# Performance work log

Measured on AMD Instinct MI355X. Metric: run time of the kernel, lower is better.

## Reference

```python
import jax, jax.numpy as jnp
import numpy as np

H = 8        # num_heads
D = 768      # d_model
DH = D // H  # d_head = 96


def setup_inputs() -> dict:
    key = jax.random.key(0)
    ks = jax.random.split(key, 12)
    B, S = 4, 2048
    s_in = 1.0 / np.sqrt(D)
    s_cat = 1.0 / np.sqrt(D)
    return {
        "input_querys": jax.random.normal(ks[0], (B, S, D), jnp.float32),
        "input_key": jax.random.normal(ks[1], (B, S, D), jnp.float32),
        "input_values": jax.random.normal(ks[2], (B, S, D), jnp.float32),
        # per-head projection weights, stacked over the head axis
        "Wq": jax.random.normal(ks[3], (H, D, DH), jnp.float32) * s_in,
        "bq": jax.random.normal(ks[4], (H, DH), jnp.float32) * s_in,
        "Wk": jax.random.normal(ks[5], (H, D, DH), jnp.float32) * s_in,
        "bk": jax.random.normal(ks[6], (H, DH), jnp.float32) * s_in,
        "Wv": jax.random.normal(ks[7], (H, D, DH), jnp.float32) * s_in,
        "bv": jax.random.normal(ks[8], (H, DH), jnp.float32) * s_in,
        # output linear: (H*DH) -> D
        "Wo": jax.random.normal(ks[9], (H * DH, D), jnp.float32) * s_cat,
        "bo": jax.random.normal(ks[10], (D,), jnp.float32) * s_cat,
    }


def reference(input_querys, input_key, input_values, Wq, bq, Wk, bk, Wv, bv, Wo, bo):
    # Per-head linear projections (vectorized over the head axis)
    # q/k/v: [B,S,D] -> [B,H,S,DH]
    Q = jnp.einsum("bsd,hdk->bhsk", input_querys, Wq) + bq[None, :, None, :]
    K = jnp.einsum("bsd,hdk->bhsk", input_key, Wk) + bk[None, :, None, :]
    V = jnp.einsum("bsd,hdk->bhsk", input_values, Wv) + bv[None, :, None, :]

    scale = 1.0 / jnp.sqrt(jnp.asarray(DH, Q.dtype))
    scores = jnp.einsum("bhsk,bhtk->bhst", Q, K) * scale  # [B,H,S,S]
    attn = jax.nn.softmax(scores, axis=-1)
    out = jnp.einsum("bhst,bhtk->bhsk", attn, V)  # [B,H,S,DH]

    # concat heads (head-major order matches torch.cat over ModuleList)
    B, _, S, _ = out.shape
    cat = out.transpose(0, 2, 1, 3).reshape(B, S, H * DH)
    return cat @ Wo + bo
```

## Files before the change

### kernel.cpp

```cpp
#include <hip/hip_runtime.h>


typedef unsigned short u16;
typedef _Float16 h16;
typedef h16 h16x8 __attribute__((ext_vector_type(8)));
typedef __fp16 fp16x2 __attribute__((ext_vector_type(2)));
typedef __fp16 fp16x4 __attribute__((ext_vector_type(4)));
typedef unsigned short u16x8 __attribute__((ext_vector_type(8)));
typedef unsigned short u16x4 __attribute__((ext_vector_type(4)));
typedef float f32x4 __attribute__((ext_vector_type(4)));

__device__ __forceinline__ u16 f2h(float f) {
  union { h16 h; u16 u; } c; c.h = (h16)f; return c.u;
}

__device__ __forceinline__ void gll16(const void* g, void* l) {
  __builtin_amdgcn_global_load_lds(
      (const __attribute__((address_space(1))) void*)g,
      (__attribute__((address_space(3))) void*)l, 16, 0, 0);
}

__global__ __launch_bounds__(256) void prep_kernel(
    const float* __restrict__ Wq, const float* __restrict__ Wk,
    const float* __restrict__ Wv, const float* __restrict__ Wo,
    const float* __restrict__ Xk, const float* __restrict__ Xv,
    const float* __restrict__ Xq,
    u16* __restrict__ WqT, u16* __restrict__ WkT,
    u16* __restrict__ WvT, u16* __restrict__ WoT,
    u16* __restrict__ Xk16, u16* __restrict__ Xv16, u16* __restrict__ Xq16)
{
  const int bid = blockIdx.x;
  const int tid = threadIdx.x;

  if (bid >= 432) {
    const int i = bid - 432;
    const int t = i / 3072;
    const long e = ((long)(i % 3072) * 256 + tid) * 8;
    const float* src = (t == 0) ? Xk : (t == 1) ? Xv : Xq;
    u16* dst = (t == 0) ? Xk16 : (t == 1) ? Xv16 : Xq16;
    f32x4 a = *(const f32x4*)(&src[e]);
    f32x4 b = *(const f32x4*)(&src[e + 4]);
    u16x8 v;
    #pragma unroll
    for (int j = 0; j < 4; j++) { v[j] = f2h(a[j]); v[4 + j] = f2h(b[j]); }
    *(u16x8*)(&dst[e]) = v;
    return;
  }

  if (bid < 288) {
    __shared__ u16 Lt[96][72];
    const int w = bid / 96;
    const int r = bid % 96;
    const int h = r / 12, dt = r % 12;
    const float* W = (w == 0) ? Wq : (w == 1) ? Wk : Wv;
    u16* T = (w == 0) ? WqT : (w == 1) ? WkT : WvT;
    const float* src = W + (size_t)h * 73728 + (size_t)dt * 64 * 96;
    #pragma unroll
    for (int p = 0; p < 6; p++) {
      const int lin = p * 1024 + tid * 4;
      f32x4 v = *(const f32x4*)(&src[lin]);
      const int d = lin / 96, kk = lin % 96;
      #pragma unroll
      for (int j = 0; j < 4; j++) Lt[kk + j][d] = f2h(v[j]);
    }
    __syncthreads();
    #pragma unroll
    for (int c = 0; c < 3; c++) {
      const int ch = c * 256 + tid;
      const int kk = ch >> 3, dc = ch & 7;
      u16x8 o = *(const u16x8*)(&Lt[kk][dc * 8]);
      *(u16x8*)(&T[(size_t)(h * 96 + kk) * 768 + dt * 64 + dc * 8]) = o;
    }
    return;
  }

  {
    __shared__ u16 Lo[64][72];
    const int i = bid - 288;
    const int kt = i / 12, nt = i % 12;
    const float* src = Wo + (size_t)(kt * 64) * 768 + nt * 64;
    #pragma unroll
    for (int p = 0; p < 4; p++) {
      const int lin = p * 1024 + tid * 4;
      const int kr = lin >> 6, nc = lin & 63;
      f32x4 v = *(const f32x4*)(&src[(size_t)kr * 768 + nc]);
      #pragma unroll
      for (int j = 0; j < 4; j++) Lo[nc + j][kr] = f2h(v[j]);
    }
    __syncthreads();
    #pragma unroll
    for (int c = 0; c < 2; c++) {
      const int ch = c * 256 + tid;
      const int nr = ch >> 3, kc = ch & 7;
      u16x8 o = *(const u16x8*)(&Lo[nr][kc * 8]);
      *(u16x8*)(&WoT[(size_t)(nt * 64 + nr) * 768 + kt * 64 + kc * 8]) = o;
    }
  }
}

#define GK 768

__global__ __launch_bounds__(256) void gemm_qkv(
    const u16* __restrict__ Xq16, const u16* __restrict__ Xk16,
    const u16* __restrict__ Xv16, const u16* __restrict__ WT,
    const float* __restrict__ bq, const float* __restrict__ bk,
    const float* __restrict__ bv,
    u16* __restrict__ Q16, u16* __restrict__ K16, u16* __restrict__ VT)
{
  const int z = blockIdx.z;
  const u16* BT = WT + (size_t)z * 589824;
  const float* bias = (z == 0) ? bq : (z == 1) ? bk : bv;
  const u16* A = (z == 0) ? Xq16 : (z == 1) ? Xk16 : Xv16;

  __shared__ __align__(16) u16 As[128 * 32];
  __shared__ __align__(16) u16 Bs[128 * 32];
  const int tid = threadIdx.x;
  const int wave = tid >> 6;
  const int lane = tid & 63;
  const int quad = lane >> 4;
  const int l16 = lane & 15;
  const int m0 = blockIdx.x * 128;
  const int n0 = blockIdx.y * 128;

  f32x4 acc[2][8];
  #pragma unroll
  for (int i = 0; i < 2; i++)
    #pragma unroll
    for (int j = 0; j < 8; j++) acc[i][j] = (f32x4){0.f, 0.f, 0.f, 0.f};

  const int Lr = lane >> 2, Lc = (lane & 3) * 8;
  const u16* gA0 = A + (size_t)(m0 + wave * 32 + Lr) * GK + Lc;
  const u16* gA1 = gA0 + (size_t)16 * GK;
  const u16* gB0 = BT + (size_t)(n0 + wave * 32 + Lr) * GK + Lc;
  const u16* gB1 = gB0 + (size_t)16 * GK;
  u16* lA0 = &As[(wave * 32) * 32];
  u16* lA1 = &As[(wave * 32 + 16) * 32];
  u16* lB0 = &Bs[(wave * 32) * 32];
  u16* lB1 = &Bs[(wave * 32 + 16) * 32];

  for (int kt = 0; kt < 24; kt++) {
    gll16(gA0, lA0);
    gll16(gA1, lA1);
    gll16(gB0, lB0);
    gll16(gB1, lB1);
    gA0 += 32; gA1 += 32; gB0 += 32; gB1 += 32;
    __syncthreads();

    h16x8 af[2], bf[8];
    #pragma unroll
    for (int mf = 0; mf < 2; mf++)
      af[mf] = *(const h16x8*)(&As[(wave * 32 + mf * 16 + l16) * 32 + quad * 8]);
    #pragma unroll
    for (int nf = 0; nf < 8; nf++)
      bf[nf] = *(const h16x8*)(&Bs[(nf * 16 + l16) * 32 + quad * 8]);
    #pragma unroll
    for (int mf = 0; mf < 2; mf++)
      #pragma unroll
      for (int nf = 0; nf < 8; nf++)
        acc[mf][nf] = __builtin_amdgcn_mfma_f32_16x16x32_f16(af[mf], bf[nf], acc[mf][nf], 0, 0, 0);
    __syncthreads();
  }

  u16* Yr = (z == 0) ? Q16 : K16;
  #pragma unroll
  for (int nf = 0; nf < 8; nf++) {
    const int n = n0 + nf * 16 + l16;
    const float bv2 = bias[n];
    #pragma unroll
    for (int mf = 0; mf < 2; mf++) {
      const int m = m0 + wave * 32 + mf * 16 + quad * 4;
      if (z == 2) {
        const int b = m >> 11, s = m & 2047;
        u16x4 pk;
        #pragma unroll
        for (int r = 0; r < 4; r++) pk[r] = f2h(acc[mf][nf][r] + bv2);
        *(u16x4*)(&VT[(size_t)b * 768 * 2048 + (size_t)n * 2048 + s]) = pk;
      } else {
        #pragma unroll
        for (int r = 0; r < 4; r++)
          Yr[(size_t)(m + r) * GK + n] = f2h(acc[mf][nf][r] + bv2);
      }
    }
  }
}

__global__ __launch_bounds__(256) void gemm_o(
    const u16* __restrict__ A, const u16* __restrict__ BT,
    const float* __restrict__ bias, float* __restrict__ Y)
{
  __shared__ __align__(16) u16 As[128 * 32];
  __shared__ __align__(16) u16 Bs[128 * 32];
  const int tid = threadIdx.x;
  const int wave = tid >> 6;
  const int lane = tid & 63;
  const int quad = lane >> 4;
  const int l16 = lane & 15;
  const int m0 = blockIdx.x * 128;
  const int n0 = blockIdx.y * 128;

  f32x4 acc[2][8];
  #pragma unroll
  for (int i = 0; i < 2; i++)
    #pragma unroll
    for (int j = 0; j < 8; j++) acc[i][j] = (f32x4){0.f, 0.f, 0.f, 0.f};

  const int Lr = lane >> 2, Lc = (lane & 3) * 8;
  const u16* gA0 = A + (size_t)(m0 + wave * 32 + Lr) * GK + Lc;
  const u16* gA1 = gA0 + (size_t)16 * GK;
  const u16* gB0 = BT + (size_t)(n0 + wave * 32 + Lr) * GK + Lc;
  const u16* gB1 = gB0 + (size_t)16 * GK;
  u16* lA0 = &As[(wave * 32) * 32];
  u16* lA1 = &As[(wave * 32 + 16) * 32];
  u16* lB0 = &Bs[(wave * 32) * 32];
  u16* lB1 = &Bs[(wave * 32 + 16) * 32];

  for (int kt = 0; kt < 24; kt++) {
    gll16(gA0, lA0);
    gll16(gA1, lA1);
    gll16(gB0, lB0);
    gll16(gB1, lB1);
    gA0 += 32; gA1 += 32; gB0 += 32; gB1 += 32;
    __syncthreads();

    h16x8 af[2], bf[8];
    #pragma unroll
    for (int mf = 0; mf < 2; mf++)
      af[mf] = *(const h16x8*)(&As[(wave * 32 + mf * 16 + l16) * 32 + quad * 8]);
    #pragma unroll
    for (int nf = 0; nf < 8; nf++)
      bf[nf] = *(const h16x8*)(&Bs[(nf * 16 + l16) * 32 + quad * 8]);
    #pragma unroll
    for (int mf = 0; mf < 2; mf++)
      #pragma unroll
      for (int nf = 0; nf < 8; nf++)
        acc[mf][nf] = __builtin_amdgcn_mfma_f32_16x16x32_f16(af[mf], bf[nf], acc[mf][nf], 0, 0, 0);
    __syncthreads();
  }

  #pragma unroll
  for (int nf = 0; nf < 8; nf++) {
    const int n = n0 + nf * 16 + l16;
    const float bv = bias[n];
    #pragma unroll
    for (int mf = 0; mf < 2; mf++) {
      const int m = m0 + wave * 32 + mf * 16 + quad * 4;
      #pragma unroll
      for (int r = 0; r < 4; r++)
        Y[(size_t)(m + r) * GK + n] = acc[mf][nf][r] + bv;
    }
  }
}

#define SEQ 2048
#define NT 32
#define LQK 104
#define LVT 72
#define LPS 72

__global__ __launch_bounds__(512, 4) void attn_kernel(
    const u16* __restrict__ Q, const u16* __restrict__ K,
    const u16* __restrict__ VT, u16* __restrict__ O)
{
  __shared__ __align__(16) u16 Ks[2][64 * LQK];
  __shared__ __align__(16) u16 Vt[2][96 * LVT];
  __shared__ __align__(16) u16 Ps[8][16 * LPS];

  const int tid = threadIdx.x;
  const int wave = tid >> 6;
  const int lane = tid & 63;
  const int quad = lane >> 4;
  const int l16 = lane & 15;

  const int bh = blockIdx.y;
  const int b = bh >> 3, h = bh & 7;
  const int q0 = blockIdx.x * 128;

  const size_t batch_off = (size_t)b * SEQ * 768;
  const u16* Kg = K + batch_off + h * 96;
  const u16* Vg = VT + (size_t)b * 768 * 2048 + (size_t)(h * 96) * 2048;

  h16x8 qf[3];
  {
    const u16* Qrow = Q + batch_off + (size_t)(q0 + wave * 16 + l16) * 768 + h * 96 + quad * 8;
    #pragma unroll
    for (int ks = 0; ks < 3; ks++) qf[ks] = *(const h16x8*)(&Qrow[ks * 32]);
  }

  const int kr0 = tid / 12, kc0 = (tid % 12) * 8;
  const int kr1 = (tid + 512) / 12, kc1 = ((tid + 512) % 12) * 8;
  const int vr0 = tid >> 3, vc0 = (tid & 7) * 8;
  const int vr1 = (tid + 512) >> 3, vc1 = ((tid + 512) & 7) * 8;
  const bool extra = tid < 256;

  f32x4 o[6];
  #pragma unroll
  for (int i = 0; i < 6; i++) o[i] = (f32x4){0.f, 0.f, 0.f, 0.f};
  float m_raw = -1e30f, lrow = 0.f;
  const float sc = 0.14724498f;

  u16* Pw = &Ps[wave][0];

  u16x8 kA, kB, vA, vB;
  kA = *(const u16x8*)(&Kg[(size_t)kr0 * 768 + kc0]);
  vA = *(const u16x8*)(&Vg[(size_t)vr0 * 2048 + vc0]);
  if (extra) {
    kB = *(const u16x8*)(&Kg[(size_t)kr1 * 768 + kc1]);
    vB = *(const u16x8*)(&Vg[(size_t)vr1 * 2048 + vc1]);
  }
  *(u16x8*)(&Ks[0][kr0 * LQK + kc0]) = kA;
  *(u16x8*)(&Vt[0][vr0 * LVT + vc0]) = vA;
  if (extra) {
    *(u16x8*)(&Ks[0][kr1 * LQK + kc1]) = kB;
    *(u16x8*)(&Vt[0][vr1 * LVT + vc1]) = vB;
  }
  {
    const u16* Kn = Kg + (size_t)64 * 768;
    const u16* Vn = Vg + 64;
    kA = *(const u16x8*)(&Kn[(size_t)kr0 * 768 + kc0]);
    vA = *(const u16x8*)(&Vn[(size_t)vr0 * 2048 + vc0]);
    if (extra) {
      kB = *(const u16x8*)(&Kn[(size_t)kr1 * 768 + kc1]);
      vB = *(const u16x8*)(&Vn[(size_t)vr1 * 2048 + vc1]);
    }
  }
  __syncthreads();

  for (int kt = 0; kt < NT; kt++) {
    const int cur = kt & 1;
    const u16* Kc = &Ks[cur][0];
    const u16* Vc = &Vt[cur][0];

    f32x4 s[4];
    #pragma unroll
    for (int kf = 0; kf < 4; kf++) s[kf] = (f32x4){0.f, 0.f, 0.f, 0.f};
    __builtin_amdgcn_s_setprio(1);
    #pragma unroll
    for (int ks = 0; ks < 3; ks++) {
      #pragma unroll
      for (int kf = 0; kf < 4; kf++) {
        h16x8 a = *(const h16x8*)(&Kc[(kf * 16 + l16) * LQK + ks * 32 + quad * 8]);
        s[kf] = __builtin_amdgcn_mfma_f32_16x16x32_f16(a, qf[ks], s[kf], 0, 0, 0);
      }
    }
    __builtin_amdgcn_s_setprio(0);

    float mx = s[0][0];
    #pragma unroll
    for (int kf = 0; kf < 4; kf++)
      #pragma unroll
      for (int r = 0; r < 4; r++) mx = fmaxf(mx, s[kf][r]);
    mx = fmaxf(mx, __shfl_xor(mx, 16));
    mx = fmaxf(mx, __shfl_xor(mx, 32));
    if (__any(mx > m_raw + 54.0f)) {
      const float mnew = fmaxf(m_raw, mx);
      const float alpha = exp2f(sc * (m_raw - mnew));
      lrow *= alpha;
      #pragma unroll
      for (int nfo = 0; nfo < 6; nfo++)
        #pragma unroll
        for (int r = 0; r < 4; r++) o[nfo][r] *= alpha;
      m_raw = mnew;
    }
    const float c0 = sc * m_raw;
    float ps = 0.f;
    #pragma unroll
    for (int kf = 0; kf < 4; kf++)
      #pragma unroll
      for (int r = 0; r < 4; r++) {
        float p = exp2f(fmaf(s[kf][r], sc, -c0));
        s[kf][r] = p;
        ps += p;
      }
    lrow += ps;

    #pragma unroll
    for (int kf = 0; kf < 4; kf++) {
      fp16x2 a2 = __builtin_amdgcn_cvt_pkrtz(s[kf][0], s[kf][1]);
      fp16x2 b2 = __builtin_amdgcn_cvt_pkrtz(s[kf][2], s[kf][3]);
      fp16x4 w4; w4[0] = a2[0]; w4[1] = a2[1]; w4[2] = b2[0]; w4[3] = b2[1];
      *(fp16x4*)(&Pw[l16 * LPS + kf * 16 + quad * 4]) = w4;
    }

    __builtin_amdgcn_s_setprio(1);
    #pragma unroll
    for (int ks = 0; ks < 2; ks++) {
      h16x8 pfr = *(const h16x8*)(&Pw[l16 * LPS + ks * 32 + quad * 8]);
      #pragma unroll
      for (int nfo = 0; nfo < 6; nfo++) {
        h16x8 vfr = *(const h16x8*)(&Vc[(nfo * 16 + l16) * LVT + ks * 32 + quad * 8]);
        o[nfo] = __builtin_amdgcn_mfma_f32_16x16x32_f16(vfr, pfr, o[nfo], 0, 0, 0);
      }
    }
    __builtin_amdgcn_s_setprio(0);

    if (kt + 1 < NT) {
      u16* Kw = &Ks[cur ^ 1][0];
      u16* Vw = &Vt[cur ^ 1][0];
      *(u16x8*)(&Kw[kr0 * LQK + kc0]) = kA;
      *(u16x8*)(&Vw[vr0 * LVT + vc0]) = vA;
      if (extra) {
        *(u16x8*)(&Kw[kr1 * LQK + kc1]) = kB;
        *(u16x8*)(&Vw[vr1 * LVT + vc1]) = vB;
      }
      if (kt + 2 < NT) {
        const u16* Kn = Kg + (size_t)(kt + 2) * 64 * 768;
        const u16* Vn = Vg + (size_t)(kt + 2) * 64;
        kA = *(const u16x8*)(&Kn[(size_t)kr0 * 768 + kc0]);
        vA = *(const u16x8*)(&Vn[(size_t)vr0 * 2048 + vc0]);
        if (extra) {
          kB = *(const u16x8*)(&Kn[(size_t)kr1 * 768 + kc1]);
          vB = *(const u16x8*)(&Vn[(size_t)vr1 * 2048 + vc1]);
        }
      }
      __syncthreads();
    }
  }

  lrow += __shfl_xor(lrow, 16);
  lrow += __shfl_xor(lrow, 32);
  const float inv = 1.0f / lrow;
  u16* Ob = O + batch_off + (size_t)(q0 + wave * 16 + l16) * 768 + h * 96;
  #pragma unroll
  for (int nfo = 0; nfo < 6; nfo++) {
    fp16x2 lo = __builtin_amdgcn_cvt_pkrtz(o[nfo][0] * inv, o[nfo][1] * inv);
    fp16x2 hi = __builtin_amdgcn_cvt_pkrtz(o[nfo][2] * inv, o[nfo][3] * inv);
    *(fp16x2*)(&Ob[nfo * 16 + quad * 4]) = lo;
    *(fp16x2*)(&Ob[nfo * 16 + quad * 4 + 2]) = hi;
  }
}

extern "C" void kernel_launch(void* const* d_in, const int* in_sizes, int n_in,
                              void* d_out, int out_size, void* d_ws, size_t ws_size,
                              hipStream_t stream) {
  const float* Xq = (const float*)d_in[0];
  const float* Xk = (const float*)d_in[1];
  const float* Xv = (const float*)d_in[2];
  const float* Wq = (const float*)d_in[3];
  const float* bq = (const float*)d_in[4];
  const float* Wk = (const float*)d_in[5];
  const float* bk = (const float*)d_in[6];
  const float* Wv = (const float*)d_in[7];
  const float* bv = (const float*)d_in[8];
  const float* Wo = (const float*)d_in[9];
  const float* bo = (const float*)d_in[10];

  u16* wsu = (u16*)d_ws;
  u16* WT   = wsu;
  u16* WoT  = wsu + 3 * 589824;
  u16* Q16  = wsu + 4 * 589824;
  u16* Xk16 = Q16 + 6291456;
  u16* Xv16 = Xk16 + 6291456;
  u16* Xq16 = Xv16 + 6291456;

  u16* outu = (u16*)d_out;
  u16* VTb = outu;
  u16* K16 = outu + 6291456;

  u16* A16 = (u16*)d_in[0];

  prep_kernel<<<9648, 256, 0, stream>>>(
      Wq, Wk, Wv, Wo, Xk, Xv, Xq,
      WT, WT + 589824, WT + 2 * 589824, WoT, Xk16, Xv16, Xq16);
  gemm_qkv<<<dim3(64, 6, 3), 256, 0, stream>>>(
      Xq16, Xk16, Xv16, WT, bq, bk, bv, Q16, K16, VTb);
  attn_kernel<<<dim3(16, 32), 512, 0, stream>>>(Q16, K16, VTb, A16);
  gemm_o<<<dim3(64, 6), 256, 0, stream>>>(A16, WoT, bo, (float*)d_out);
}
```

Before: 291.8 us.

## Deepen GEMM K-tiles with swizzled LDS, stage V transpose, software-pipeline attention QK^T

Both projection GEMMs now load 64-wide K tiles with an XOR-swizzled LDS layout, halving barrier count and avoiding bank conflicts. The V projection's transposed output is staged through shared memory so global stores become contiguous 16-byte rows instead of scattered 4-element writes. The attention kernel is restructured so the QK^T MFMAs for the next tile are issued before the softmax/PV of the current tile, overlapping matrix work with exponentials, at the cost of more registers and extra barriers.

```diff
diff --git a/kernel.cpp b/kernel.cpp
--- a/kernel.cpp
+++ b/kernel.cpp
@@ -112,8 +112,10 @@
   const float* bias = (z == 0) ? bq : (z == 1) ? bk : bv;
   const u16* A = (z == 0) ? Xq16 : (z == 1) ? Xk16 : Xv16;
 
-  __shared__ __align__(16) u16 As[128 * 32];
-  __shared__ __align__(16) u16 Bs[128 * 32];
+  __shared__ __align__(16) u16 S[16384];
+  u16* As = S;
+  u16* Bs = S + 8192;
+
   const int tid = threadIdx.x;
   const int wave = tid >> 6;
   const int lane = tid & 63;
@@ -128,37 +130,73 @@
     #pragma unroll
     for (int j = 0; j < 8; j++) acc[i][j] = (f32x4){0.f, 0.f, 0.f, 0.f};
 
-  const int Lr = lane >> 2, Lc = (lane & 3) * 8;
-  const u16* gA0 = A + (size_t)(m0 + wave * 32 + Lr) * GK + Lc;
-  const u16* gA1 = gA0 + (size_t)16 * GK;
-  const u16* gB0 = BT + (size_t)(n0 + wave * 32 + Lr) * GK + Lc;
-  const u16* gB1 = gB0 + (size_t)16 * GK;
-  u16* lA0 = &As[(wave * 32) * 32];
-  u16* lA1 = &As[(wave * 32 + 16) * 32];
-  u16* lB0 = &Bs[(wave * 32) * 32];
-  u16* lB1 = &Bs[(wave * 32 + 16) * 32];
-
-  for (int kt = 0; kt < 24; kt++) {
-    gll16(gA0, lA0);
-    gll16(gA1, lA1);
-    gll16(gB0, lB0);
-    gll16(gB1, lB1);
-    gA0 += 32; gA1 += 32; gB0 += 32; gB1 += 32;
-    __syncthreads();
-
-    h16x8 af[2], bf[8];
-    #pragma unroll
-    for (int mf = 0; mf < 2; mf++)
-      af[mf] = *(const h16x8*)(&As[(wave * 32 + mf * 16 + l16) * 32 + quad * 8]);
-    #pragma unroll
-    for (int nf = 0; nf < 8; nf++)
-      bf[nf] = *(const h16x8*)(&Bs[(nf * 16 + l16) * 32 + quad * 8]);
-    #pragma unroll
-    for (int mf = 0; mf < 2; mf++)
+  int srow[4], scol[4];
+  #pragma unroll
+  for (int p = 0; p < 4; p++) {
+    const int c = p * 256 + tid;
+    srow[p] = c >> 3;
+    scol[p] = ((c & 7) ^ (srow[p] & 7)) << 3;
+  }
+  const int x7 = (l16 & 7) << 3;
+
+  for (int kt = 0; kt < 12; kt++) {
+    const int k0 = kt * 64;
+    #pragma unroll
+    for (int p = 0; p < 4; p++) {
+      gll16(&A[(size_t)(m0 + srow[p]) * GK + k0 + scol[p]],
+            As + (size_t)(p * 256 + wave * 64) * 8);
+      gll16(&BT[(size_t)(n0 + srow[p]) * GK + k0 + scol[p]],
+            Bs + (size_t)(p * 256 + wave * 64) * 8);
+    }
+    __syncthreads();
+
+    #pragma unroll
+    for (int ks2 = 0; ks2 < 2; ks2++) {
+      const int cc = (ks2 * 32 + quad * 8) ^ x7;
+      h16x8 af[2], bf[8];
+      #pragma unroll
+      for (int mf = 0; mf < 2; mf++)
+        af[mf] = *(const h16x8*)(&As[(wave * 32 + mf * 16 + l16) * 64 + cc]);
       #pragma unroll
       for (int nf = 0; nf < 8; nf++)
-        acc[mf][nf] = __builtin_amdgcn_mfma_f32_16x16x32_f16(af[mf], bf[nf], acc[mf][nf], 0, 0, 0);
-    __syncthreads();
+        bf[nf] = *(const h16x8*)(&Bs[(nf * 16 + l16) * 64 + cc]);
+      #pragma unroll
+      for (int mf = 0; mf < 2; mf++)
+        #pragma unroll
+        for (int nf = 0; nf < 8; nf++)
+          acc[mf][nf] = __builtin_amdgcn_mfma_f32_16x16x32_f16(af[mf], bf[nf], acc[mf][nf], 0, 0, 0);
+    }
+    __syncthreads();
+  }
+
+  if (z == 2) {
+    const int b = m0 >> 11, s0 = m0 & 2047;
+    u16* Ts = S;
+    #pragma unroll
+    for (int half = 0; half < 2; half++) {
+      __syncthreads();
+      #pragma unroll
+      for (int nf2 = 0; nf2 < 4; nf2++) {
+        const int nf = half * 4 + nf2;
+        const float bv2 = bias[n0 + nf * 16 + l16];
+        #pragma unroll
+        for (int mf = 0; mf < 2; mf++)
+          #pragma unroll
+          for (int r = 0; r < 4; r++)
+            Ts[(nf2 * 16 + l16) * 136 + wave * 32 + mf * 16 + quad * 4 + r] =
+                f2h(acc[mf][nf][r] + bv2);
+      }
+      __syncthreads();
+      #pragma unroll
+      for (int p = 0; p < 4; p++) {
+        const int c = p * 256 + tid;
+        const int row = c >> 4, col8 = (c & 15) * 8;
+        u16x8 o8 = *(const u16x8*)(&Ts[row * 136 + col8]);
+        *(u16x8*)(&VT[(size_t)b * 768 * 2048 +
+                      (size_t)(n0 + half * 64 + row) * 2048 + s0 + col8]) = o8;
+      }
+    }
+    return;
   }
 
   u16* Yr = (z == 0) ? Q16 : K16;
@@ -169,17 +207,9 @@
     #pragma unroll
     for (int mf = 0; mf < 2; mf++) {
       const int m = m0 + wave * 32 + mf * 16 + quad * 4;
-      if (z == 2) {
-        const int b = m >> 11, s = m & 2047;
-        u16x4 pk;
-        #pragma unroll
-        for (int r = 0; r < 4; r++) pk[r] = f2h(acc[mf][nf][r] + bv2);
-        *(u16x4*)(&VT[(size_t)b * 768 * 2048 + (size_t)n * 2048 + s]) = pk;
-      } else {
-        #pragma unroll
-        for (int r = 0; r < 4; r++)
-          Yr[(size_t)(m + r) * GK + n] = f2h(acc[mf][nf][r] + bv2);
-      }
+      #pragma unroll
+      for (int r = 0; r < 4; r++)
+        Yr[(size_t)(m + r) * GK + n] = f2h(acc[mf][nf][r] + bv2);
     }
   }
 }
@@ -188,8 +218,10 @@
     const u16* __restrict__ A, const u16* __restrict__ BT,
     const float* __restrict__ bias, float* __restrict__ Y)
 {
-  __shared__ __align__(16) u16 As[128 * 32];
-  __shared__ __align__(16) u16 Bs[128 * 32];
+  __shared__ __align__(16) u16 S[16384];
+  u16* As = S;
+  u16* Bs = S + 8192;
+
   const int tid = threadIdx.x;
   const int wave = tid >> 6;
   const int lane = tid & 63;
@@ -204,36 +236,42 @@
     #pragma unroll
     for (int j = 0; j < 8; j++) acc[i][j] = (f32x4){0.f, 0.f, 0.f, 0.f};
 
-  const int Lr = lane >> 2, Lc = (lane & 3) * 8;
-  const u16* gA0 = A + (size_t)(m0 + wave * 32 + Lr) * GK + Lc;
-  const u16* gA1 = gA0 + (size_t)16 * GK;
-  const u16* gB0 = BT + (size_t)(n0 + wave * 32 + Lr) * GK + Lc;
-  const u16* gB1 = gB0 + (size_t)16 * GK;
-  u16* lA0 = &As[(wave * 32) * 32];
-  u16* lA1 = &As[(wave * 32 + 16) * 32];
-  u16* lB0 = &Bs[(wave * 32) * 32];
-  u16* lB1 = &Bs[(wave * 32 + 16) * 32];
-
-  for (int kt = 0; kt < 24; kt++) {
-    gll16(gA0, lA0);
-    gll16(gA1, lA1);
-    gll16(gB0, lB0);
-    gll16(gB1, lB1);
-    gA0 += 32; gA1 += 32; gB0 += 32; gB1 += 32;
-    __syncthreads();
-
-    h16x8 af[2], bf[8];
-    #pragma unroll
-    for (int mf = 0; mf < 2; mf++)
-      af[mf] = *(const h16x8*)(&As[(wave * 32 + mf * 16 + l16) * 32 + quad * 8]);
-    #pragma unroll
-    for (int nf = 0; nf < 8; nf++)
-      bf[nf] = *(const h16x8*)(&Bs[(nf * 16 + l16) * 32 + quad * 8]);
-    #pragma unroll
-    for (int mf = 0; mf < 2; mf++)
+  int srow[4], scol[4];
+  #pragma unroll
+  for (int p = 0; p < 4; p++) {
+    const int c = p * 256 + tid;
+    srow[p] = c >> 3;
+    scol[p] = ((c & 7) ^ (srow[p] & 7)) << 3;
+  }
+  const int x7 = (l16 & 7) << 3;
+
+  for (int kt = 0; kt < 12; kt++) {
+    const int k0 = kt * 64;
+    #pragma unroll
+    for (int p = 0; p < 4; p++) {
+      gll16(&A[(size_t)(m0 + srow[p]) * GK + k0 + scol[p]],
+            As + (size_t)(p * 256 + wave * 64) * 8);
+      gll16(&BT[(size_t)(n0 + srow[p]) * GK + k0 + scol[p]],
+            Bs + (size_t)(p * 256 + wave * 64) * 8);
+    }
+    __syncthreads();
+
+    #pragma unroll
+    for (int ks2 = 0; ks2 < 2; ks2++) {
+      const int cc = (ks2 * 32 + quad * 8) ^ x7;
+      h16x8 af[2], bf[8];
+      #pragma unroll
+      for (int mf = 0; mf < 2; mf++)
+        af[mf] = *(const h16x8*)(&As[(wave * 32 + mf * 16 + l16) * 64 + cc]);
       #pragma unroll
       for (int nf = 0; nf < 8; nf++)
-        acc[mf][nf] = __builtin_amdgcn_mfma_f32_16x16x32_f16(af[mf], bf[nf], acc[mf][nf], 0, 0, 0);
+        bf[nf] = *(const h16x8*)(&Bs[(nf * 16 + l16) * 64 + cc]);
+      #pragma unroll
+      for (int mf = 0; mf < 2; mf++)
+        #pragma unroll
+        for (int nf = 0; nf < 8; nf++)
+          acc[mf][nf] = __builtin_amdgcn_mfma_f32_16x16x32_f16(af[mf], bf[nf], acc[mf][nf], 0, 0, 0);
+    }
     __syncthreads();
   }
 
@@ -301,36 +339,26 @@
   u16* Pw = &Ps[wave][0];
 
   u16x8 kA, kB, vA, vB;
-  kA = *(const u16x8*)(&Kg[(size_t)kr0 * 768 + kc0]);
-  vA = *(const u16x8*)(&Vg[(size_t)vr0 * 2048 + vc0]);
-  if (extra) {
-    kB = *(const u16x8*)(&Kg[(size_t)kr1 * 768 + kc1]);
-    vB = *(const u16x8*)(&Vg[(size_t)vr1 * 2048 + vc1]);
-  }
-  *(u16x8*)(&Ks[0][kr0 * LQK + kc0]) = kA;
-  *(u16x8*)(&Vt[0][vr0 * LVT + vc0]) = vA;
-  if (extra) {
-    *(u16x8*)(&Ks[0][kr1 * LQK + kc1]) = kB;
-    *(u16x8*)(&Vt[0][vr1 * LVT + vc1]) = vB;
-  }
-  {
-    const u16* Kn = Kg + (size_t)64 * 768;
-    const u16* Vn = Vg + 64;
+
+  auto load_tile = [&](int t) {
+    const u16* Kn = Kg + (size_t)t * 64 * 768;
+    const u16* Vn = Vg + (size_t)t * 64;
     kA = *(const u16x8*)(&Kn[(size_t)kr0 * 768 + kc0]);
     vA = *(const u16x8*)(&Vn[(size_t)vr0 * 2048 + vc0]);
     if (extra) {
       kB = *(const u16x8*)(&Kn[(size_t)kr1 * 768 + kc1]);
       vB = *(const u16x8*)(&Vn[(size_t)vr1 * 2048 + vc1]);
     }
-  }
-  __syncthreads();
-
-  for (int kt = 0; kt < NT; kt++) {
-    const int cur = kt & 1;
-    const u16* Kc = &Ks[cur][0];
-    const u16* Vc = &Vt[cur][0];
-
-    f32x4 s[4];
+  };
+  auto stage_write = [&](int buf) {
+    *(u16x8*)(&Ks[buf][kr0 * LQK + kc0]) = kA;
+    *(u16x8*)(&Vt[buf][vr0 * LVT + vc0]) = vA;
+    if (extra) {
+      *(u16x8*)(&Ks[buf][kr1 * LQK + kc1]) = kB;
+      *(u16x8*)(&Vt[buf][vr1 * LVT + vc1]) = vB;
+    }
+  };
+  auto qkt = [&](f32x4 (&s)[4], const u16* Kc) {
     #pragma unroll
     for (int kf = 0; kf < 4; kf++) s[kf] = (f32x4){0.f, 0.f, 0.f, 0.f};
     __builtin_amdgcn_s_setprio(1);
@@ -343,7 +371,8 @@
       }
     }
     __builtin_amdgcn_s_setprio(0);
-
+  };
+  auto process = [&](f32x4 (&s)[4], const u16* Vc) {
     float mx = s[0][0];
     #pragma unroll
     for (int kf = 0; kf < 4; kf++)
@@ -372,7 +401,6 @@
         ps += p;
       }
     lrow += ps;
-
     #pragma unroll
     for (int kf = 0; kf < 4; kf++) {
       fp16x2 a2 = __builtin_amdgcn_cvt_pkrtz(s[kf][0], s[kf][1]);
@@ -380,7 +408,6 @@
       fp16x4 w4; w4[0] = a2[0]; w4[1] = a2[1]; w4[2] = b2[0]; w4[3] = b2[1];
       *(fp16x4*)(&Pw[l16 * LPS + kf * 16 + quad * 4]) = w4;
     }
-
     __builtin_amdgcn_s_setprio(1);
     #pragma unroll
     for (int ks = 0; ks < 2; ks++) {
@@ -392,29 +419,33 @@
       }
     }
     __builtin_amdgcn_s_setprio(0);
-
-    if (kt + 1 < NT) {
-      u16* Kw = &Ks[cur ^ 1][0];
-      u16* Vw = &Vt[cur ^ 1][0];
-      *(u16x8*)(&Kw[kr0 * LQK + kc0]) = kA;
-      *(u16x8*)(&Vw[vr0 * LVT + vc0]) = vA;
-      if (extra) {
-        *(u16x8*)(&Kw[kr1 * LQK + kc1]) = kB;
-        *(u16x8*)(&Vw[vr1 * LVT + vc1]) = vB;
-      }
-      if (kt + 2 < NT) {
-        const u16* Kn = Kg + (size_t)(kt + 2) * 64 * 768;
-        const u16* Vn = Vg + (size_t)(kt + 2) * 64;
-        kA = *(const u16x8*)(&Kn[(size_t)kr0 * 768 + kc0]);
-        vA = *(const u16x8*)(&Vn[(size_t)vr0 * 2048 + vc0]);
-        if (extra) {
-          kB = *(const u16x8*)(&Kn[(size_t)kr1 * 768 + kc1]);
-          vB = *(const u16x8*)(&Vn[(size_t)vr1 * 2048 + vc1]);
-        }
-      }
-      __syncthreads();
-    }
-  }
+  };
+
+  load_tile(0); stage_write(0);
+  load_tile(1); stage_write(1);
+  load_tile(2);
+  __syncthreads();
+
+  f32x4 sA[4], sB[4];
+  qkt(sA, &Ks[0][0]);
+
+  for (int t = 1; t < NT - 1; t += 2) {
+    qkt(sB, &Ks[1][0]);
+    process(sA, &Vt[0][0]);
+    __syncthreads();
+    stage_write(0);
+    if (t + 2 < NT) load_tile(t + 2);
+    __syncthreads();
+    qkt(sA, &Ks[0][0]);
+    process(sB, &Vt[1][0]);
+    __syncthreads();
+    stage_write(1);
+    if (t + 3 < NT) load_tile(t + 3);
+    __syncthreads();
+  }
+  qkt(sB, &Ks[1][0]);
+  process(sA, &Vt[0][0]);
+  process(sB, &Vt[1][0]);
 
   lrow += __shfl_xor(lrow, 16);
   lrow += __shfl_xor(lrow, 32);
```

Result: slower. 315.5 us (+8.1%).
